# Optimization experiments

Hardware: AMD Instinct MI355X
Metric: run time of the kernel (lower is better)

The kernel has to match this reference:

```python
import jax, jax.numpy as jnp
import numpy as np

B, D, E, H, L = 32768, 512, 10, 128, 2  # batch, input_dim, max_charts, expert hidden, latent_dim
RH1, RH2 = 256, 128                      # router hidden sizes
TAU = 3.0


def setup_inputs() -> dict:
    key = jax.random.key(0)
    ks = jax.random.split(key, 16)
    rnd = lambda k, *s: (jax.random.normal(k, s, jnp.float32) * 0.05)
    return {
        "x": jax.random.normal(ks[0], (B, D), jnp.float32),
        "u": jax.random.uniform(ks[1], (B, E), jnp.float32),
        # router params (last layer init ~ N(0, 0.01), bias 0, as in _init_router)
        "rw1": rnd(ks[2], D, RH1), "rb1": jnp.zeros((RH1,), jnp.float32),
        "rw2": rnd(ks[3], RH1, RH2), "rb2": jnp.zeros((RH2,), jnp.float32),
        "rw3": jax.random.normal(ks[4], (RH2, E), jnp.float32) * 0.01,
        "rb3": jnp.zeros((E,), jnp.float32),
        # stacked expert params: all 10 experts batched along leading dim
        "ew1": rnd(ks[5], E, D, H), "eb1": rnd(ks[6], E, H),
        "ew2": rnd(ks[7], E, H, H), "eb2": rnd(ks[8], E, H),
        "ew3": rnd(ks[9], E, H, L), "eb3": rnd(ks[10], E, L),
    }


def reference(x, u, rw1, rb1, rw2, rb2, rw3, rb3, ew1, eb1, ew2, eb2, ew3, eb3):
    # router MLP: D -> 256 -> 128 -> E
    h = jax.nn.relu(x @ rw1 + rb1)
    h = jax.nn.relu(h @ rw2 + rb2)
    logits = h @ rw3 + rb3                                  # [B, E]
    # gumbel_softmax(tau=3.0, hard=False): softmax((logits + gumbel)/tau)
    g = -jnp.log(-jnp.log(jnp.clip(u, 1e-10, 1.0)) + 1e-10)
    weights = jax.nn.softmax((logits + g) / TAU, axis=1)    # [B, E]
    # all 10 experts as batched GEMMs (fuses the python loop over charts)
    h1 = jax.nn.relu(jnp.einsum('bi,eio->beo', x, ew1) + eb1[None])   # [B, E, H]
    h2 = jax.nn.relu(jnp.einsum('beh,eho->beo', h1, ew2) + eb2[None]) # [B, E, H]
    zc = jnp.einsum('beh,ehl->bel', h2, ew3) + eb3[None]              # [B, E, L]
    z = jnp.einsum('be,bel->bl', weights, zc)                         # [B, L]
    chart_outputs = jnp.transpose(zc, (1, 0, 2))                      # [E, B, L]
    return z, weights, chart_outputs
```

## Files before the change

kernel.cpp:

```cpp
#include <hip/hip_runtime.h>
#include <stdint.h>

typedef __bf16 bf16x8 __attribute__((ext_vector_type(8)));
typedef float floatx4 __attribute__((ext_vector_type(4)));
typedef unsigned short ushort_t;

__device__ __forceinline__ ushort_t bf16rne(float f) {
    union { float f; unsigned u; } v; v.f = f;
    return (ushort_t)((v.u + 0x7fffu + ((v.u >> 16) & 1u)) >> 16);
}

__device__ __forceinline__ void gl_lds16(const ushort_t* g, ushort_t* l) {
    __builtin_amdgcn_global_load_lds(
        (const __attribute__((address_space(1))) unsigned int*)g,
        (__attribute__((address_space(3))) unsigned int*)l, 16, 0, 0);
}


__global__ void prep(const float* __restrict__ x, ushort_t* __restrict__ x16,
                     const float* __restrict__ ew1, ushort_t* __restrict__ ew1t,
                     const float* __restrict__ ew2, ushort_t* __restrict__ ew2t,
                     const float* __restrict__ rw1, ushort_t* __restrict__ rw1t,
                     const float* __restrict__ rw2, ushort_t* __restrict__ rw2t) {
    __shared__ ushort_t sT[64 * 65];
    int b = blockIdx.x, tid = threadIdx.x;
    if (b < 16384) {
        int i = b * 256 + tid;
        float4 f = ((const float4*)x)[i];
        union { ushort_t s[4]; uint2 v; } pk;
        pk.s[0] = bf16rne(f.x); pk.s[1] = bf16rne(f.y);
        pk.s[2] = bf16rne(f.z); pk.s[3] = bf16rne(f.w);
        ((uint2*)x16)[i] = pk.v;
        return;
    }
    const float* in; ushort_t* outp; int K, N, k0, n0;
    int i = b - 16384;
    if (i < 160) {
        int e = i >> 4, t = i & 15;
        in = ew1 + e * 65536; outp = ew1t + e * 65536;
        K = 512; N = 128; k0 = (t >> 1) * 64; n0 = (t & 1) * 64;
    } else if (i < 200) {
        i -= 160; int e = i >> 2, t = i & 3;
        in = ew2 + e * 16384; outp = ew2t + e * 16384;
        K = 128; N = 128; k0 = (t >> 1) * 64; n0 = (t & 1) * 64;
    } else if (i < 232) {
        i -= 200; in = rw1; outp = rw1t;
        K = 512; N = 256; k0 = (i >> 2) * 64; n0 = (i & 3) * 64;
    } else {
        i -= 232; in = rw2; outp = rw2t;
        K = 256; N = 128; k0 = (i >> 1) * 64; n0 = (i & 1) * 64;
    }
    {
        int c = tid & 63, r0 = tid >> 6;
#pragma unroll
        for (int p = 0; p < 16; ++p) {
            int r = r0 * 16 + p;
            sT[c * 65 + r] = bf16rne(in[(size_t)(k0 + r) * N + n0 + c]);
        }
        __syncthreads();
        int rr = tid & 63, c0 = tid >> 6;
#pragma unroll
        for (int p = 0; p < 16; ++p) {
            int cc = c0 * 16 + p;
            outp[(size_t)(n0 + cc) * K + k0 + rr] = sT[cc * 65 + rr];
        }
    }
}

__global__ __launch_bounds__(256, 2)
void fused_main(const ushort_t* __restrict__ x16,
                const ushort_t* __restrict__ rw1t, const float* __restrict__ rb1,
                const ushort_t* __restrict__ rw2t, const float* __restrict__ rb2,
                const float* __restrict__ rw3, const float* __restrict__ rb3,
                const float* __restrict__ u,
                const ushort_t* __restrict__ ew1t, const ushort_t* __restrict__ ew2t,
                const float* __restrict__ eb1, const float* __restrict__ eb2,
                const float* __restrict__ ew3, const float* __restrict__ eb3,
                float* __restrict__ wts, float* __restrict__ chart) {
    __shared__ alignas(16) ushort_t sU[24576];
    __shared__ float sB1[2][128];
    __shared__ float sB2[2][128];
    __shared__ float sW3e[2][256];
    __shared__ float zbuf[128][2];

    const int tid = threadIdx.x;
    const int id = blockIdx.x;
    const int wave = tid >> 6, lane = tid & 63;
    const int ln15 = lane & 15, q = lane >> 4;
    const int wm = (wave & 1) * 64, wn = (wave >> 1) * 64;
    const int mhalf = wm >> 6, nhalf = wn >> 6;
    const int rl = lane >> 2, cl = lane & 3;
    const int sw = (cl ^ ((rl >> 1) & 3)) * 8;
    const int rg0 = wave * 2, rg1 = rg0 + 1;
    const int fslot = (4 * ln15 + (q ^ ((ln15 >> 1) & 3))) * 8;

    if (id < 256) {
        const int rb = (id & 7) * 32 + (id >> 3);
        if (tid < 128) sB2[0][tid] = rb2[tid];
        else sB2[1][tid - 128] = rb2[tid];
        const ushort_t* xblk = x16 + (size_t)rb * 128 * 512;

        floatx4 acc2[4][4];
#pragma unroll
        for (int i = 0; i < 4; ++i)
#pragma unroll
            for (int j = 0; j < 4; ++j) acc2[i][j] = (floatx4){0.f, 0.f, 0.f, 0.f};

        for (int ph = 0; ph < 2; ++ph) {
            if (tid < 128) sB1[0][tid] = rb1[ph * 128 + tid];
            const ushort_t* w1base = rw1t + (size_t)ph * 128 * 512;

            floatx4 acc[4][4];
#pragma unroll
            for (int i = 0; i < 4; ++i)
#pragma unroll
                for (int j = 0; j < 4; ++j) acc[i][j] = (floatx4){0.f, 0.f, 0.f, 0.f};

            for (int k0 = 0; k0 < 512; k0 += 32) {
                __syncthreads();
                gl_lds16(xblk + (size_t)(rg0 * 16 + rl) * 512 + k0 + sw, &sU[rg0 * 512]);
                gl_lds16(xblk + (size_t)(rg1 * 16 + rl) * 512 + k0 + sw, &sU[rg1 * 512]);
                gl_lds16(w1base + (size_t)(rg0 * 16 + rl) * 512 + k0 + sw, &sU[4096 + rg0 * 512]);
                gl_lds16(w1base + (size_t)(rg1 * 16 + rl) * 512 + k0 + sw, &sU[4096 + rg1 * 512]);
                __syncthreads();
                bf16x8 a[4], b[4];
#pragma unroll
                for (int t = 0; t < 4; ++t) a[t] = *(const bf16x8*)(&sU[4096 + (mhalf * 4 + t) * 512 + fslot]);
#pragma unroll
                for (int t = 0; t < 4; ++t) b[t] = *(const bf16x8*)(&sU[(nhalf * 4 + t) * 512 + fslot]);
#pragma unroll
                for (int i = 0; i < 4; ++i)
#pragma unroll
                    for (int j = 0; j < 4; ++j)
                        acc[i][j] = __builtin_amdgcn_mfma_f32_16x16x32_bf16(a[i], b[j], acc[i][j], 0, 0, 0);
            }

#pragma unroll
            for (int i = 0; i < 4; ++i) {
                int hbase = wm + 16 * i;
                int kh = hbase >> 5;
                int qhi = (hbase >> 4) & 1;
                int slotq = 2 * qhi + (q >> 1);
                int h0 = hbase + q * 4;
#pragma unroll
                for (int j = 0; j < 4; ++j) {
                    union { ushort_t s[4]; uint2 v; } pk;
#pragma unroll
                    for (int r = 0; r < 4; ++r)
                        pk.s[r] = bf16rne(fmaxf(acc[i][j][r] + sB1[0][h0 + r], 0.f));
                    *(uint2*)(&sU[8192 + kh * 4096 + (nhalf * 4 + j) * 512 + slotq * 128 + ln15 * 8 + (q & 1) * 4]) = pk.v;
                }
            }

            for (int p = 0; p < 2; ++p) {
                __syncthreads();
#pragma unroll
                for (int r = 0; r < 4; ++r) {
                    int s = wave * 4 + r;
                    int khl = s >> 3, rg = s & 7;
                    int kh = p * 2 + khl;
                    gl_lds16(rw2t + (size_t)(rg * 16 + rl) * 256 + ph * 128 + kh * 32 + sw, &sU[s * 512]);
                }
                __syncthreads();
#pragma unroll
                for (int khl = 0; khl < 2; ++khl) {
                    int kh = p * 2 + khl;
                    bf16x8 a[4], b[4];
#pragma unroll
                    for (int t = 0; t < 4; ++t) a[t] = *(const bf16x8*)(&sU[(khl * 8 + mhalf * 4 + t) * 512 + fslot]);
#pragma unroll
                    for (int t = 0; t < 4; ++t) b[t] = *(const bf16x8*)(&sU[8192 + kh * 4096 + (nhalf * 4 + t) * 512 + lane * 8]);
#pragma unroll
                    for (int i = 0; i < 4; ++i)
#pragma unroll
                        for (int j = 0; j < 4; ++j)
                            acc2[i][j] = __builtin_amdgcn_mfma_f32_16x16x32_bf16(a[i], b[j], acc2[i][j], 0, 0, 0);
                }
            }
        }

        __syncthreads();
        float* sw3r = (float*)sU;
        float* lgbuf = (float*)(&sU[2560]);
        for (int i = tid; i < 1280; i += 256) sw3r[i] = rw3[i];
        __syncthreads();

        float lg[4][10];
#pragma unroll
        for (int j = 0; j < 4; ++j)
#pragma unroll
            for (int ee = 0; ee < 10; ++ee) lg[j][ee] = 0.f;
#pragma unroll
        for (int i = 0; i < 4; ++i) {
#pragma unroll
            for (int r = 0; r < 4; ++r) {
                int n = wm + i * 16 + q * 4 + r;
                float bias = n < 128 ? sB2[0][n] : sB2[1][n - 128];
                const float* w3r = &sw3r[n * 10];
#pragma unroll
                for (int j = 0; j < 4; ++j) {
                    float val = fmaxf(acc2[i][j][r] + bias, 0.f);
#pragma unroll
                    for (int ee = 0; ee < 10; ++ee) lg[j][ee] += val * w3r[ee];
                }
            }
        }
#pragma unroll
        for (int j = 0; j < 4; ++j)
#pragma unroll
            for (int ee = 0; ee < 10; ++ee) {
                lg[j][ee] += __shfl_xor(lg[j][ee], 16, 64);
                lg[j][ee] += __shfl_xor(lg[j][ee], 32, 64);
            }
        if (wm == 0 && q == 0) {
#pragma unroll
            for (int j = 0; j < 4; ++j) {
                int row = wn + 16 * j + ln15;
#pragma unroll
                for (int ee = 0; ee < 10; ++ee) lgbuf[row * 10 + ee] = lg[j][ee];
            }
        }
        __syncthreads();
        if (wm == 64 && q == 0) {
#pragma unroll
            for (int j = 0; j < 4; ++j) {
                int row = wn + 16 * j + ln15;
#pragma unroll
                for (int ee = 0; ee < 10; ++ee) lgbuf[row * 10 + ee] += lg[j][ee];
            }
        }
        __syncthreads();
        if (tid < 128) {
            int grow = rb * 128 + tid;
            float v[10], mx = -1e30f;
#pragma unroll
            for (int ee = 0; ee < 10; ++ee) {
                float uu = u[(size_t)grow * 10 + ee];
                uu = fminf(fmaxf(uu, 1e-10f), 1.0f);
                float g = -logf(-logf(uu) + 1e-10f);
                v[ee] = (lgbuf[tid * 10 + ee] + rb3[ee] + g) * (1.0f / 3.0f);
                mx = fmaxf(mx, v[ee]);
            }
            float s = 0.f;
#pragma unroll
            for (int ee = 0; ee < 10; ++ee) { v[ee] = expf(v[ee] - mx); s += v[ee]; }
            float inv = 1.0f / s;
#pragma unroll
            for (int ee = 0; ee < 10; ++ee) wts[(size_t)grow * 10 + ee] = v[ee] * inv;
        }
    } else {
        const int eid = id - 256;
        const int xcd = eid & 7, local = eid >> 3;
        const int pr = local % 5;
        const int rb = xcd * 32 + local / 5;
        const int e0 = pr * 2;

        if (tid < 128) {
            sB1[0][tid] = eb1[e0 * 128 + tid];
            sB2[0][tid] = eb2[e0 * 128 + tid];
        } else {
            sB1[1][tid - 128] = eb1[(e0 + 1) * 128 + (tid - 128)];
            sB2[1][tid - 128] = eb2[(e0 + 1) * 128 + (tid - 128)];
        }
        sW3e[0][tid] = ew3[e0 * 256 + tid];
        sW3e[1][tid] = ew3[(e0 + 1) * 256 + tid];

        const ushort_t* xblk = x16 + (size_t)rb * 128 * 512;
        const ushort_t* w1a = ew1t + (size_t)e0 * 65536;
        const ushort_t* w1b = w1a + 65536;

        floatx4 accA[4][4], accB[4][4];
#pragma unroll
        for (int i = 0; i < 4; ++i)
#pragma unroll
            for (int j = 0; j < 4; ++j) {
                accA[i][j] = (floatx4){0.f, 0.f, 0.f, 0.f};
                accB[i][j] = (floatx4){0.f, 0.f, 0.f, 0.f};
            }

        for (int k0 = 0; k0 < 512; k0 += 32) {
            __syncthreads();
            gl_lds16(xblk + (size_t)(rg0 * 16 + rl) * 512 + k0 + sw, &sU[rg0 * 512]);
            gl_lds16(xblk + (size_t)(rg1 * 16 + rl) * 512 + k0 + sw, &sU[rg1 * 512]);
            gl_lds16(w1a + (size_t)(rg0 * 16 + rl) * 512 + k0 + sw, &sU[4096 + rg0 * 512]);
            gl_lds16(w1a + (size_t)(rg1 * 16 + rl) * 512 + k0 + sw, &sU[4096 + rg1 * 512]);
            gl_lds16(w1b + (size_t)(rg0 * 16 + rl) * 512 + k0 + sw, &sU[8192 + rg0 * 512]);
            gl_lds16(w1b + (size_t)(rg1 * 16 + rl) * 512 + k0 + sw, &sU[8192 + rg1 * 512]);
            __syncthreads();
            bf16x8 a0[4], a1[4], b[4];
#pragma unroll
            for (int t = 0; t < 4; ++t) b[t] = *(const bf16x8*)(&sU[(nhalf * 4 + t) * 512 + fslot]);
#pragma unroll
            for (int t = 0; t < 4; ++t) a0[t] = *(const bf16x8*)(&sU[4096 + (mhalf * 4 + t) * 512 + fslot]);
#pragma unroll
            for (int t = 0; t < 4; ++t) a1[t] = *(const bf16x8*)(&sU[8192 + (mhalf * 4 + t) * 512 + fslot]);
#pragma unroll
            for (int i = 0; i < 4; ++i)
#pragma unroll
                for (int j = 0; j < 4; ++j) {
                    accA[i][j] = __builtin_amdgcn_mfma_f32_16x16x32_bf16(a0[i], b[j], accA[i][j], 0, 0, 0);
                    accB[i][j] = __builtin_amdgcn_mfma_f32_16x16x32_bf16(a1[i], b[j], accB[i][j], 0, 0, 0);
                }
        }
        __syncthreads();

#pragma unroll
        for (int ex = 0; ex < 2; ++ex) {
            const int e = e0 + ex;
            const ushort_t* w2 = ew2t + (size_t)e * 16384;

#pragma unroll
            for (int i = 0; i < 4; ++i) {
                int hbase = wm + 16 * i;
                int kh = hbase >> 5;
                int qhi = (hbase >> 4) & 1;
                int slotq = 2 * qhi + (q >> 1);
                int h0 = hbase + q * 4;
#pragma unroll
                for (int j = 0; j < 4; ++j) {
                    union { ushort_t s[4]; uint2 v; } pk;
#pragma unroll
                    for (int r = 0; r < 4; ++r) {
                        float av = ex == 0 ? accA[i][j][r] : accB[i][j][r];
                        pk.s[r] = bf16rne(fmaxf(av + sB1[ex][h0 + r], 0.f));
                    }
                    *(uint2*)(&sU[8192 + kh * 4096 + (nhalf * 4 + j) * 512 + slotq * 128 + ln15 * 8 + (q & 1) * 4]) = pk.v;
                }
            }

            floatx4 acc2[4][4];
#pragma unroll
            for (int i = 0; i < 4; ++i)
#pragma unroll
                for (int j = 0; j < 4; ++j) acc2[i][j] = (floatx4){0.f, 0.f, 0.f, 0.f};

            for (int p = 0; p < 2; ++p) {
                __syncthreads();
#pragma unroll
                for (int r = 0; r < 4; ++r) {
                    int s = wave * 4 + r;
                    int khl = s >> 3, rg = s & 7;
                    int kh = p * 2 + khl;
                    gl_lds16(w2 + (size_t)(rg * 16 + rl) * 128 + kh * 32 + sw, &sU[s * 512]);
                }
                __syncthreads();
#pragma unroll
                for (int khl = 0; khl < 2; ++khl) {
                    int kh = p * 2 + khl;
                    bf16x8 a[4], b[4];
#pragma unroll
                    for (int t = 0; t < 4; ++t) a[t] = *(const bf16x8*)(&sU[(khl * 8 + mhalf * 4 + t) * 512 + fslot]);
#pragma unroll
                    for (int t = 0; t < 4; ++t) b[t] = *(const bf16x8*)(&sU[8192 + kh * 4096 + (nhalf * 4 + t) * 512 + lane * 8]);
#pragma unroll
                    for (int i = 0; i < 4; ++i)
#pragma unroll
                        for (int j = 0; j < 4; ++j)
                            acc2[i][j] = __builtin_amdgcn_mfma_f32_16x16x32_bf16(a[i], b[j], acc2[i][j], 0, 0, 0);
                }
            }

            float zc0[4] = {0.f, 0.f, 0.f, 0.f}, zc1[4] = {0.f, 0.f, 0.f, 0.f};
#pragma unroll
            for (int i = 0; i < 4; ++i) {
                int o0 = wm + i * 16 + q * 4;
#pragma unroll
                for (int r = 0; r < 4; ++r) {
                    int o = o0 + r;
                    float w3a = sW3e[ex][2 * o], w3b = sW3e[ex][2 * o + 1];
                    float bias = sB2[ex][o];
#pragma unroll
                    for (int j = 0; j < 4; ++j) {
                        float val = fmaxf(acc2[i][j][r] + bias, 0.f);
                        zc0[j] += val * w3a;
                        zc1[j] += val * w3b;
                    }
                }
            }
#pragma unroll
            for (int j = 0; j < 4; ++j) {
                zc0[j] += __shfl_xor(zc0[j], 16, 64);
                zc0[j] += __shfl_xor(zc0[j], 32, 64);
                zc1[j] += __shfl_xor(zc1[j], 16, 64);
                zc1[j] += __shfl_xor(zc1[j], 32, 64);
            }
            if (wm == 0 && q == 0) {
#pragma unroll
                for (int j = 0; j < 4; ++j) {
                    int row = wn + j * 16 + ln15;
                    zbuf[row][0] = zc0[j];
                    zbuf[row][1] = zc1[j];
                }
            }
            __syncthreads();
            if (wm == 64 && q == 0) {
#pragma unroll
                for (int j = 0; j < 4; ++j) {
                    int row = wn + j * 16 + ln15;
                    zbuf[row][0] += zc0[j];
                    zbuf[row][1] += zc1[j];
                }
            }
            __syncthreads();
            {
                int row = tid >> 1, l = tid & 1;
                int grow = rb * 128 + row;
                chart[(size_t)e * 65536 + (size_t)grow * 2 + l] = zbuf[row][l] + eb3[e * 2 + l];
            }
        }
    }
}

__global__ void z_final(const float* __restrict__ w, const float* __restrict__ chart,
                        float* __restrict__ z) {
    int row = blockIdx.x * 256 + threadIdx.x;
    float z0 = 0.f, z1 = 0.f;
#pragma unroll
    for (int e = 0; e < 10; ++e) {
        float we = w[(size_t)row * 10 + e];
        float2 c = *(const float2*)(&chart[(size_t)e * 65536 + (size_t)row * 2]);
        z0 += we * c.x;
        z1 += we * c.y;
    }
    float2 o; o.x = z0; o.y = z1;
    *(float2*)(&z[(size_t)row * 2]) = o;
}

extern "C" void kernel_launch(void* const* d_in, const int* in_sizes, int n_in,
                              void* d_out, int out_size, void* d_ws, size_t ws_size,
                              hipStream_t stream) {
    const float* x = (const float*)d_in[0];
    const float* u = (const float*)d_in[1];
    const float* rw1 = (const float*)d_in[2];
    const float* rb1 = (const float*)d_in[3];
    const float* rw2 = (const float*)d_in[4];
    const float* rb2 = (const float*)d_in[5];
    const float* rw3 = (const float*)d_in[6];
    const float* rb3 = (const float*)d_in[7];
    const float* ew1 = (const float*)d_in[8];
    const float* eb1 = (const float*)d_in[9];
    const float* ew2 = (const float*)d_in[10];
    const float* eb2 = (const float*)d_in[11];
    const float* ew3 = (const float*)d_in[12];
    const float* eb3 = (const float*)d_in[13];
    float* out = (float*)d_out;
    float* z = out;
    float* wts = out + 65536;
    float* chart = out + 393216;

    ushort_t* x16  = (ushort_t*)d_ws;
    ushort_t* ew1t = x16 + 16777216;
    ushort_t* ew2t = ew1t + 655360;
    ushort_t* rw1t = ew2t + 163840;
    ushort_t* rw2t = rw1t + 131072;

    prep<<<16624, 256, 0, stream>>>(x, x16, ew1, ew1t, ew2, ew2t, rw1, rw1t, rw2, rw2t);

    fused_main<<<1536, 256, 0, stream>>>(x16, rw1t, rb1, rw2t, rb2, rw3, rb3, u,
                                         ew1t, ew2t, eb1, eb2, ew3, eb3,
                                         wts, chart);

    z_final<<<128, 256, 0, stream>>>(wts, chart, z);
}
```

Before: 211.3 us.

## Double-buffer LDS staging with async loads and vmcnt-based waits in MLP GEMMs

Replaces the load-sync-compute-sync loops in the router and expert GEMMs with a two-stage ping-pong LDS pipeline. The next K-slice is issued through global_load_lds while the current one is consumed, and full __syncthreads is swapped for explicit s_waitcnt vmcnt/lgkmcnt plus s_barrier. The second-layer weight loads are split into per-kh stages that are prefetched during the bf16 store of the previous activations. s_setprio is raised around the MFMA blocks. The aim is to hide global-memory latency behind matrix math. The cost is more LDS use and reliance on hand-counted vmcnt values, which must match the number of outstanding loads per wave.

```diff
diff --git a/kernel.cpp b/kernel.cpp
--- a/kernel.cpp
+++ b/kernel.cpp
@@ -16,6 +16,10 @@
         (__attribute__((address_space(3))) unsigned int*)l, 16, 0, 0);
 }
 
+
+#define WAIT_VM_BAR(n)    do { asm volatile("s_waitcnt vmcnt(" #n ")" ::: "memory"); __builtin_amdgcn_s_barrier(); } while (0)
+#define WAIT_VM_LG_BAR(n) do { asm volatile("s_waitcnt vmcnt(" #n ") lgkmcnt(0)" ::: "memory"); __builtin_amdgcn_s_barrier(); } while (0)
+#define WAIT_LG_BAR()     do { asm volatile("s_waitcnt lgkmcnt(0)" ::: "memory"); __builtin_amdgcn_s_barrier(); } while (0)
 
 __global__ void prep(const float* __restrict__ x, ushort_t* __restrict__ x16,
                      const float* __restrict__ ew1, ushort_t* __restrict__ ew1t,
@@ -100,15 +104,46 @@
         else sB2[1][tid - 128] = rb2[tid];
         const ushort_t* xblk = x16 + (size_t)rb * 128 * 512;
 
+        const ushort_t* w1base = rw1t;
+        auto stage_rt = [&](int dst, int k0) {
+            gl_lds16(xblk + (size_t)(rg0 * 16 + rl) * 512 + k0 + sw, &sU[dst + rg0 * 512]);
+            gl_lds16(xblk + (size_t)(rg1 * 16 + rl) * 512 + k0 + sw, &sU[dst + rg1 * 512]);
+            gl_lds16(w1base + (size_t)(rg0 * 16 + rl) * 512 + k0 + sw, &sU[dst + 4096 + rg0 * 512]);
+            gl_lds16(w1base + (size_t)(rg1 * 16 + rl) * 512 + k0 + sw, &sU[dst + 4096 + rg1 * 512]);
+        };
+        auto stage_rw2 = [&](int dst, int kh, int ph) {
+#pragma unroll
+            for (int r = 0; r < 2; ++r) {
+                int s = wave * 2 + r;
+                gl_lds16(rw2t + (size_t)(s * 16 + rl) * 256 + ph * 128 + kh * 32 + sw,
+                         &sU[dst + s * 512]);
+            }
+        };
+
         floatx4 acc2[4][4];
 #pragma unroll
         for (int i = 0; i < 4; ++i)
 #pragma unroll
             for (int j = 0; j < 4; ++j) acc2[i][j] = (floatx4){0.f, 0.f, 0.f, 0.f};
 
+        auto comp_rg2 = [&](int rbase, int kh) {
+            bf16x8 a[4], b[4];
+#pragma unroll
+            for (int t = 0; t < 4; ++t) a[t] = *(const bf16x8*)(&sU[rbase + (mhalf * 4 + t) * 512 + fslot]);
+#pragma unroll
+            for (int t = 0; t < 4; ++t) b[t] = *(const bf16x8*)(&sU[8192 + kh * 4096 + (nhalf * 4 + t) * 512 + lane * 8]);
+            __builtin_amdgcn_s_setprio(1);
+#pragma unroll
+            for (int i = 0; i < 4; ++i)
+#pragma unroll
+                for (int j = 0; j < 4; ++j)
+                    acc2[i][j] = __builtin_amdgcn_mfma_f32_16x16x32_bf16(a[i], b[j], acc2[i][j], 0, 0, 0);
+            __builtin_amdgcn_s_setprio(0);
+        };
+
         for (int ph = 0; ph < 2; ++ph) {
+            w1base = rw1t + (size_t)ph * 65536;
             if (tid < 128) sB1[0][tid] = rb1[ph * 128 + tid];
-            const ushort_t* w1base = rw1t + (size_t)ph * 128 * 512;
 
             floatx4 acc[4][4];
 #pragma unroll
@@ -116,24 +151,40 @@
 #pragma unroll
                 for (int j = 0; j < 4; ++j) acc[i][j] = (floatx4){0.f, 0.f, 0.f, 0.f};
 
-            for (int k0 = 0; k0 < 512; k0 += 32) {
-                __syncthreads();
-                gl_lds16(xblk + (size_t)(rg0 * 16 + rl) * 512 + k0 + sw, &sU[rg0 * 512]);
-                gl_lds16(xblk + (size_t)(rg1 * 16 + rl) * 512 + k0 + sw, &sU[rg1 * 512]);
-                gl_lds16(w1base + (size_t)(rg0 * 16 + rl) * 512 + k0 + sw, &sU[4096 + rg0 * 512]);
-                gl_lds16(w1base + (size_t)(rg1 * 16 + rl) * 512 + k0 + sw, &sU[4096 + rg1 * 512]);
-                __syncthreads();
+            auto comp_rt = [&](int base) {
                 bf16x8 a[4], b[4];
 #pragma unroll
-                for (int t = 0; t < 4; ++t) a[t] = *(const bf16x8*)(&sU[4096 + (mhalf * 4 + t) * 512 + fslot]);
-#pragma unroll
-                for (int t = 0; t < 4; ++t) b[t] = *(const bf16x8*)(&sU[(nhalf * 4 + t) * 512 + fslot]);
+                for (int t = 0; t < 4; ++t) a[t] = *(const bf16x8*)(&sU[base + 4096 + (mhalf * 4 + t) * 512 + fslot]);
+#pragma unroll
+                for (int t = 0; t < 4; ++t) b[t] = *(const bf16x8*)(&sU[base + (nhalf * 4 + t) * 512 + fslot]);
+                __builtin_amdgcn_s_setprio(1);
 #pragma unroll
                 for (int i = 0; i < 4; ++i)
 #pragma unroll
                     for (int j = 0; j < 4; ++j)
                         acc[i][j] = __builtin_amdgcn_mfma_f32_16x16x32_bf16(a[i], b[j], acc[i][j], 0, 0, 0);
-            }
+                __builtin_amdgcn_s_setprio(0);
+            };
+
+            stage_rt(0, 0);
+#pragma unroll 1
+            for (int p = 0; p < 8; ++p) {
+                int k0 = p * 64;
+                stage_rt(8192, k0 + 32);
+                WAIT_VM_BAR(4);
+                comp_rt(0);
+                WAIT_LG_BAR();
+                if (p < 7) {
+                    stage_rt(0, k0 + 64);
+                    WAIT_VM_BAR(4);
+                } else {
+                    WAIT_VM_BAR(0);
+                }
+                comp_rt(8192);
+                WAIT_LG_BAR();
+            }
+
+            stage_rw2(0, 0, ph);
 
 #pragma unroll
             for (int i = 0; i < 4; ++i) {
@@ -152,31 +203,10 @@
                 }
             }
 
-            for (int p = 0; p < 2; ++p) {
-                __syncthreads();
-#pragma unroll
-                for (int r = 0; r < 4; ++r) {
-                    int s = wave * 4 + r;
-                    int khl = s >> 3, rg = s & 7;
-                    int kh = p * 2 + khl;
-                    gl_lds16(rw2t + (size_t)(rg * 16 + rl) * 256 + ph * 128 + kh * 32 + sw, &sU[s * 512]);
-                }
-                __syncthreads();
-#pragma unroll
-                for (int khl = 0; khl < 2; ++khl) {
-                    int kh = p * 2 + khl;
-                    bf16x8 a[4], b[4];
-#pragma unroll
-                    for (int t = 0; t < 4; ++t) a[t] = *(const bf16x8*)(&sU[(khl * 8 + mhalf * 4 + t) * 512 + fslot]);
-#pragma unroll
-                    for (int t = 0; t < 4; ++t) b[t] = *(const bf16x8*)(&sU[8192 + kh * 4096 + (nhalf * 4 + t) * 512 + lane * 8]);
-#pragma unroll
-                    for (int i = 0; i < 4; ++i)
-#pragma unroll
-                        for (int j = 0; j < 4; ++j)
-                            acc2[i][j] = __builtin_amdgcn_mfma_f32_16x16x32_bf16(a[i], b[j], acc2[i][j], 0, 0, 0);
-                }
-            }
+            stage_rw2(4096, 1, ph); WAIT_VM_LG_BAR(8); comp_rg2(0, 0);    WAIT_LG_BAR();
+            stage_rw2(0, 2, ph);    WAIT_VM_LG_BAR(8); comp_rg2(4096, 1); WAIT_LG_BAR();
+            stage_rw2(4096, 3, ph); WAIT_VM_LG_BAR(8); comp_rg2(0, 2);    WAIT_LG_BAR();
+            WAIT_VM_LG_BAR(0);                         comp_rg2(4096, 3); WAIT_LG_BAR();
         }
 
         __syncthreads();
@@ -278,22 +308,23 @@
                 accB[i][j] = (floatx4){0.f, 0.f, 0.f, 0.f};
             }
 
-        for (int k0 = 0; k0 < 512; k0 += 32) {
-            __syncthreads();
-            gl_lds16(xblk + (size_t)(rg0 * 16 + rl) * 512 + k0 + sw, &sU[rg0 * 512]);
-            gl_lds16(xblk + (size_t)(rg1 * 16 + rl) * 512 + k0 + sw, &sU[rg1 * 512]);
-            gl_lds16(w1a + (size_t)(rg0 * 16 + rl) * 512 + k0 + sw, &sU[4096 + rg0 * 512]);
-            gl_lds16(w1a + (size_t)(rg1 * 16 + rl) * 512 + k0 + sw, &sU[4096 + rg1 * 512]);
-            gl_lds16(w1b + (size_t)(rg0 * 16 + rl) * 512 + k0 + sw, &sU[8192 + rg0 * 512]);
-            gl_lds16(w1b + (size_t)(rg1 * 16 + rl) * 512 + k0 + sw, &sU[8192 + rg1 * 512]);
-            __syncthreads();
+        auto stage_g1 = [&](int dst, int k0) {
+            gl_lds16(xblk + (size_t)(rg0 * 16 + rl) * 512 + k0 + sw, &sU[dst + rg0 * 512]);
+            gl_lds16(xblk + (size_t)(rg1 * 16 + rl) * 512 + k0 + sw, &sU[dst + rg1 * 512]);
+            gl_lds16(w1a + (size_t)(rg0 * 16 + rl) * 512 + k0 + sw, &sU[dst + 4096 + rg0 * 512]);
+            gl_lds16(w1a + (size_t)(rg1 * 16 + rl) * 512 + k0 + sw, &sU[dst + 4096 + rg1 * 512]);
+            gl_lds16(w1b + (size_t)(rg0 * 16 + rl) * 512 + k0 + sw, &sU[dst + 8192 + rg0 * 512]);
+            gl_lds16(w1b + (size_t)(rg1 * 16 + rl) * 512 + k0 + sw, &sU[dst + 8192 + rg1 * 512]);
+        };
+        auto comp_g1 = [&](int base) {
             bf16x8 a0[4], a1[4], b[4];
 #pragma unroll
-            for (int t = 0; t < 4; ++t) b[t] = *(const bf16x8*)(&sU[(nhalf * 4 + t) * 512 + fslot]);
-#pragma unroll
-            for (int t = 0; t < 4; ++t) a0[t] = *(const bf16x8*)(&sU[4096 + (mhalf * 4 + t) * 512 + fslot]);
-#pragma unroll
-            for (int t = 0; t < 4; ++t) a1[t] = *(const bf16x8*)(&sU[8192 + (mhalf * 4 + t) * 512 + fslot]);
+            for (int t = 0; t < 4; ++t) b[t] = *(const bf16x8*)(&sU[base + (nhalf * 4 + t) * 512 + fslot]);
+#pragma unroll
+            for (int t = 0; t < 4; ++t) a0[t] = *(const bf16x8*)(&sU[base + 4096 + (mhalf * 4 + t) * 512 + fslot]);
+#pragma unroll
+            for (int t = 0; t < 4; ++t) a1[t] = *(const bf16x8*)(&sU[base + 8192 + (mhalf * 4 + t) * 512 + fslot]);
+            __builtin_amdgcn_s_setprio(1);
 #pragma unroll
             for (int i = 0; i < 4; ++i)
 #pragma unroll
@@ -301,13 +332,55 @@
                     accA[i][j] = __builtin_amdgcn_mfma_f32_16x16x32_bf16(a0[i], b[j], accA[i][j], 0, 0, 0);
                     accB[i][j] = __builtin_amdgcn_mfma_f32_16x16x32_bf16(a1[i], b[j], accB[i][j], 0, 0, 0);
                 }
-        }
-        __syncthreads();
+            __builtin_amdgcn_s_setprio(0);
+        };
+
+        stage_g1(0, 0);
+#pragma unroll 1
+        for (int p = 0; p < 8; ++p) {
+            int k0 = p * 64;
+            stage_g1(12288, k0 + 32);
+            WAIT_VM_BAR(6);
+            comp_g1(0);
+            WAIT_LG_BAR();
+            if (p < 7) {
+                stage_g1(0, k0 + 64);
+                WAIT_VM_BAR(6);
+            } else {
+                WAIT_VM_BAR(0);
+            }
+            comp_g1(12288);
+            WAIT_LG_BAR();
+        }
+
+        auto stage_w2 = [&](const ushort_t* w2, int dst, int kh) {
+#pragma unroll
+            for (int r = 0; r < 2; ++r) {
+                int s = wave * 2 + r;
+                gl_lds16(w2 + (size_t)(s * 16 + rl) * 128 + kh * 32 + sw, &sU[dst + s * 512]);
+            }
+        };
+        auto comp_g2 = [&](int rbase, int kh, floatx4 (&acc2)[4][4]) {
+            bf16x8 a[4], b[4];
+#pragma unroll
+            for (int t = 0; t < 4; ++t) a[t] = *(const bf16x8*)(&sU[rbase + (mhalf * 4 + t) * 512 + fslot]);
+#pragma unroll
+            for (int t = 0; t < 4; ++t) b[t] = *(const bf16x8*)(&sU[8192 + kh * 4096 + (nhalf * 4 + t) * 512 + lane * 8]);
+            __builtin_amdgcn_s_setprio(1);
+#pragma unroll
+            for (int i = 0; i < 4; ++i)
+#pragma unroll
+                for (int j = 0; j < 4; ++j)
+                    acc2[i][j] = __builtin_amdgcn_mfma_f32_16x16x32_bf16(a[i], b[j], acc2[i][j], 0, 0, 0);
+            __builtin_amdgcn_s_setprio(0);
+        };
 
 #pragma unroll
         for (int ex = 0; ex < 2; ++ex) {
             const int e = e0 + ex;
             const ushort_t* w2 = ew2t + (size_t)e * 16384;
+
+            stage_w2(w2, 0, 0);
 
 #pragma unroll
             for (int i = 0; i < 4; ++i) {
@@ -334,31 +407,10 @@
 #pragma unroll
                 for (int j = 0; j < 4; ++j) acc2[i][j] = (floatx4){0.f, 0.f, 0.f, 0.f};
 
-            for (int p = 0; p < 2; ++p) {
-                __syncthreads();
-#pragma unroll
-                for (int r = 0; r < 4; ++r) {
-                    int s = wave * 4 + r;
-                    int khl = s >> 3, rg = s & 7;
-                    int kh = p * 2 + khl;
-                    gl_lds16(w2 + (size_t)(rg * 16 + rl) * 128 + kh * 32 + sw, &sU[s * 512]);
-                }
-                __syncthreads();
-#pragma unroll
-                for (int khl = 0; khl < 2; ++khl) {
-                    int kh = p * 2 + khl;
-                    bf16x8 a[4], b[4];
-#pragma unroll
-                    for (int t = 0; t < 4; ++t) a[t] = *(const bf16x8*)(&sU[(khl * 8 + mhalf * 4 + t) * 512 + fslot]);
-#pragma unroll
-                    for (int t = 0; t < 4; ++t) b[t] = *(const bf16x8*)(&sU[8192 + kh * 4096 + (nhalf * 4 + t) * 512 + lane * 8]);
-#pragma unroll
-                    for (int i = 0; i < 4; ++i)
-#pragma unroll
-                        for (int j = 0; j < 4; ++j)
-                            acc2[i][j] = __builtin_amdgcn_mfma_f32_16x16x32_bf16(a[i], b[j], acc2[i][j], 0, 0, 0);
-                }
-            }
+            stage_w2(w2, 4096, 1); WAIT_VM_LG_BAR(8); comp_g2(0, 0, acc2);    WAIT_LG_BAR();
+            stage_w2(w2, 0, 2);    WAIT_VM_LG_BAR(8); comp_g2(4096, 1, acc2); WAIT_LG_BAR();
+            stage_w2(w2, 4096, 3); WAIT_VM_LG_BAR(8); comp_g2(0, 2, acc2);    WAIT_LG_BAR();
+            WAIT_VM_LG_BAR(0);                        comp_g2(4096, 3, acc2); WAIT_LG_BAR();
 
             float zc0[4] = {0.f, 0.f, 0.f, 0.f}, zc1[4] = {0.f, 0.f, 0.f, 0.f};
 #pragma unroll
```

Measured after the change: 204.4 us. 1.03x faster.
